# Kernel tuning notes

Hardware: AMD Instinct MI355X
Metric: run time of the kernel (lower is better)

## Reference

```python
import jax, jax.numpy as jnp
import numpy as np

B, S, IN, HID, OUT = 8, 4096, 128, 128, 1

def setup_inputs() -> dict:
    key = jax.random.key(0)
    ks = jax.random.split(key, 16)
    xav = lambda k, i, o: jax.random.normal(k, (i, o), jnp.float32) * np.sqrt(2.0 / (i + o))
    return {
        'x': jax.random.normal(ks[0], (B, S, IN), jnp.float32),
        'm1': xav(ks[1], IN, HID), 'b1': jnp.zeros((1, 1, HID), jnp.float32),
        'm2': xav(ks[2], HID, HID), 'b2': jnp.zeros((1, 1, HID), jnp.float32),
        'wq': xav(ks[3], HID, HID), 'wk': xav(ks[4], HID, HID), 'wv': xav(ks[5], HID, HID),
        'ml0': xav(ks[6], 128, 64), 'bl0': jnp.zeros((1, 1, 64), jnp.float32),
        'ml1': xav(ks[7], 64, 32), 'bl1': jnp.zeros((1, 1, 32), jnp.float32),
        'm3': xav(ks[8], 32, OUT), 'b3': jnp.zeros((1, 1, OUT), jnp.float32),
        'atten_size': 5,
    }

def reference(x, m1, b1, m2, b2, wq, wk, wv, ml0, bl0, ml1, bl1, m3, b3, atten_size):
    a = atten_size
    h = jax.nn.relu(x @ m1 + b1)
    h = jax.nn.relu(h @ m2 + b2)            # [B,S,H]
    vals = h @ wv
    pad_cfg = ((0, 0), (a, a), (0, 0))
    padded = jnp.pad(h, pad_cfg)
    padded_v = jnp.pad(vals, pad_cfg)
    # window gather via roll, matching torch.roll(padded, k, 1) for k=-a..a, then slice
    x_nei = jnp.stack([jnp.roll(padded, k, axis=1) for k in range(-a, a + 1)], axis=2)[:, a:-a]   # [B,S,W,H]
    v_nei = jnp.stack([jnp.roll(padded_v, k, axis=1) for k in range(-a, a + 1)], axis=2)[:, a:-a]
    keys = x_nei @ wk                        # [B,S,W,H]
    query = h @ wq                           # [B,S,H]
    scale = 1.0 / np.sqrt(float(HID))
    dot = jnp.einsum('bswh,bsh->bsw', keys, query) * scale
    atten_w = jax.nn.softmax(dot, axis=2)    # [B,S,W]
    o = jnp.einsum('bsw,bswh->bsh', atten_w, v_nei)
    o = jax.nn.relu(o @ ml0 + bl0)
    o = jax.nn.relu(o @ ml1 + bl1)
    o = jax.nn.sigmoid(o @ m3 + b3)          # [B,S,OUT]
    return (o, atten_w)
```

## Files before the change

kernel.cpp:

```cpp
#include <hip/hip_runtime.h>
#include <hip/hip_bf16.h>
#include <math.h>

#define SEQ 4096
#define NB 8
#define CHUNK 64
#define HALO 5
#define WIN 11
#define MROWS 80
#define AROWS 74
#define HSTR 136
#define NT 512
#define CNT 256

typedef short s16x8 __attribute__((ext_vector_type(8)));
typedef float f32x4 __attribute__((ext_vector_type(4)));

__device__ __forceinline__ unsigned short f2bf(float f) {
    return __builtin_bit_cast(unsigned short, __float2bfloat16(f));
}

#define OFF_M1  0
#define OFF_M2  16384
#define OFF_WQK 32768
#define OFF_WF  49152
#define OFF_ML1 57344
#define WS_ELEMS 59392

__global__ void convert_weights(const float* __restrict__ m1, const float* __restrict__ m2,
                                const float* __restrict__ wq, const float* __restrict__ wk,
                                const float* __restrict__ wv, const float* __restrict__ ml0,
                                const float* __restrict__ ml1, unsigned short* __restrict__ ws)
{
    int idx = blockIdx.x * CNT + threadIdx.x;
    if (idx < 16384) {
        ws[idx] = f2bf(m1[(idx & 127) * 128 + (idx >> 7)]);
    } else if (idx < 32768) {
        int r = idx - 16384;
        ws[idx] = f2bf(m2[(r & 127) * 128 + (r >> 7)]);
    } else if (idx < 49152) {
        int r = idx - 32768;
        int d = r >> 7, e = r & 127;
        const float4* qa = (const float4*)(wq + e * 128);
        const float4* ka = (const float4*)(wk + d * 128);
        float a0 = 0.f, a1 = 0.f, a2 = 0.f, a3 = 0.f;
        #pragma unroll
        for (int c = 0; c < 32; ++c) {
            float4 A = qa[c], B = ka[c];
            a0 = fmaf(A.x, B.x, a0); a1 = fmaf(A.y, B.y, a1);
            a2 = fmaf(A.z, B.z, a2); a3 = fmaf(A.w, B.w, a3);
        }
        ws[idx] = f2bf((a0 + a1 + a2 + a3) * 0.08838834764831845f);
    } else if (idx < 57344) {
        int r = idx - 49152;
        int n = r >> 7, k = r & 127;
        const float* vr = wv + k * 128;
        float a = 0.f;
        #pragma unroll
        for (int c = 0; c < 128; ++c) a = fmaf(vr[c], ml0[c * 64 + n], a);
        ws[idx] = f2bf(a);
    } else if (idx < WS_ELEMS) {
        int r = idx - 57344;
        int n = r >> 6, k = r & 63;
        ws[idx] = f2bf(ml1[k * 32 + n]);
    }
}

__device__ __forceinline__ void loadB4(s16x8 d[4], const unsigned short* __restrict__ wt,
                                       int ct, int l15, int hi)
{
    const unsigned short* p = wt + (ct * 16 + l15) * 128 + hi * 8;
    d[0] = *(const s16x8*)(p);
    d[1] = *(const s16x8*)(p + 32);
    d[2] = *(const s16x8*)(p + 64);
    d[3] = *(const s16x8*)(p + 96);
}

template<int MT, bool RELU, bool BIAS>
__device__ __forceinline__ void gemmS(const unsigned short* __restrict__ src,
                                      const s16x8 bf[4],
                                      const float* __restrict__ bias,
                                      unsigned short* __restrict__ dst,
                                      int l15, int hi, int wave)
{
    f32x4 acc[MT];
    #pragma unroll
    for (int i = 0; i < MT; ++i) acc[i] = (f32x4){0.f, 0.f, 0.f, 0.f};
    const unsigned short* arow = src + l15 * HSTR + hi * 8;
    #pragma unroll
    for (int ks = 0; ks < 4; ++ks)
        #pragma unroll
        for (int rt = 0; rt < MT; ++rt) {
            s16x8 a = *(const s16x8*)(arow + rt * 16 * HSTR + ks * 32);
            acc[rt] = __builtin_amdgcn_mfma_f32_16x16x32_bf16(a, bf[ks], acc[rt], 0, 0, 0);
        }
    const int c = wave * 16 + l15;
    const float bb = BIAS ? bias[c] : 0.f;
    #pragma unroll
    for (int rt = 0; rt < MT; ++rt)
        #pragma unroll
        for (int j = 0; j < 4; ++j) {
            float v = acc[rt][j] + bb;
            if (RELU) v = fmaxf(v, 0.f);
            dst[(rt * 16 + hi * 4 + j) * HSTR + c] = f2bf(v);
        }
}

__global__ __launch_bounds__(NT, 4)
void ExLRestSelfAtten_mfma(const float* __restrict__ x,
                           const float* __restrict__ b1, const float* __restrict__ b2,
                           const float* __restrict__ bl0, const float* __restrict__ bl1,
                           const float* __restrict__ m3, const float* __restrict__ b3,
                           const unsigned short* __restrict__ wsw,
                           float* __restrict__ out0, float* __restrict__ attw)
{
    __shared__ __align__(16) unsigned short bufA[MROWS * HSTR];
    __shared__ __align__(16) unsigned short bufB[MROWS * HSTR];
    __shared__ __align__(16) unsigned short qbuf[CHUNK * HSTR];
    __shared__ __align__(16) float sbuf[4 * 16 * 36];
    __shared__ __align__(16) float saw [CHUNK * WIN];

    unsigned short* o2b  = bufA;
    float*          fbuf = (float*)qbuf;

    const int t = threadIdx.x;
    const int lane = t & 63, wave = t >> 6;
    const int l15 = lane & 15, hi = lane >> 4;
    const int bx = blockIdx.x;
    const int b = bx >> 6;
    const int cstart = (bx & 63) * CHUNK;

    s16x8 wA[4], wB[4], wml1[2];
    loadB4(wA, wsw + OFF_M1, wave, l15, hi);

    const float* xb = x + (size_t)b * SEQ * 128;
    for (int idx = t; idx < MROWS * 32; idx += NT) {
        int r = idx >> 5, k4 = (idx & 31) << 2;
        int p = cstart - HALO + r;
        float4 v = make_float4(0.f, 0.f, 0.f, 0.f);
        if (r < AROWS && p >= 0 && p < SEQ) v = *(const float4*)(xb + (size_t)p * 128 + k4);
        ushort4 o;
        o.x = f2bf(v.x); o.y = f2bf(v.y); o.z = f2bf(v.z); o.w = f2bf(v.w);
        *(ushort4*)(bufA + r * HSTR + k4) = o;
    }
    __syncthreads();

    loadB4(wB, wsw + OFF_M2, wave, l15, hi);
    gemmS<5, true, true>(bufA, wA, b1, bufB, l15, hi, wave);
    __syncthreads();

    loadB4(wA, wsw + OFF_WQK, wave, l15, hi);
    gemmS<5, true, true>(bufB, wB, b2, bufA, l15, hi, wave);
    __syncthreads();

    loadB4(wB, wsw + OFF_WF, wave & 3, l15, hi);
    gemmS<4, false, false>(bufA + HALO * HSTR, wA, nullptr, qbuf, l15, hi, wave);
    {
        const int cg = wave & 3, rh = wave >> 2;
        const int rt0 = rh ? 3 : 0, ntr = rh ? 2 : 3;
        f32x4 acc[3];
        #pragma unroll
        for (int i = 0; i < 3; ++i) acc[i] = (f32x4){0.f, 0.f, 0.f, 0.f};
        const unsigned short* arow = bufA + (rt0 * 16 + l15) * HSTR + hi * 8;
        #pragma unroll
        for (int ks = 0; ks < 4; ++ks)
            for (int rt = 0; rt < ntr; ++rt) {
                s16x8 a = *(const s16x8*)(arow + rt * 16 * HSTR + ks * 32);
                acc[rt] = __builtin_amdgcn_mfma_f32_16x16x32_bf16(a, wB[ks], acc[rt], 0, 0, 0);
            }
        const int c = cg * 16 + l15;
        for (int rt = 0; rt < ntr; ++rt)
            #pragma unroll
            for (int j = 0; j < 4; ++j)
                bufB[((rt0 + rt) * 16 + hi * 4 + j) * HSTR + c] = f2bf(acc[rt][j]);
    }
    __syncthreads();

    {
        const unsigned short* p1 = wsw + OFF_ML1 + ((wave & 1) * 16 + l15) * 64 + hi * 8;
        wml1[0] = *(const s16x8*)(p1);
        wml1[1] = *(const s16x8*)(p1 + 32);
    }
    {
        const int rt = wave >> 1, kk = wave & 1, kt = rt + kk;
        f32x4 sacc = (f32x4){0.f, 0.f, 0.f, 0.f};
        #pragma unroll
        for (int ks = 0; ks < 4; ++ks) {
            s16x8 a  = *(const s16x8*)(qbuf + (rt * 16 + l15) * HSTR + ks * 32 + hi * 8);
            s16x8 hb = *(const s16x8*)(bufA + (kt * 16 + l15) * HSTR + ks * 32 + hi * 8);
            sacc = __builtin_amdgcn_mfma_f32_16x16x32_bf16(a, hb, sacc, 0, 0, 0);
        }
        #pragma unroll
        for (int j = 0; j < 4; ++j)
            sbuf[rt * 576 + (hi * 4 + j) * 36 + kk * 16 + l15] = sacc[j];
    }
    __syncthreads();

    if (t < CHUNK) {
        const int base = (t >> 4) * 576 + (t & 15) * 36 + (t & 15) + 10;
        float d[WIN], mx = -1e30f;
        #pragma unroll
        for (int w = 0; w < WIN; ++w) { d[w] = sbuf[base - w]; mx = fmaxf(mx, d[w]); }
        float sum = 0.f;
        #pragma unroll
        for (int w = 0; w < WIN; ++w) { d[w] = __expf(d[w] - mx); sum += d[w]; }
        float inv = 1.f / sum;
        float* ab = attw + (size_t)(b * SEQ + cstart + t) * WIN;
        #pragma unroll
        for (int w = 0; w < WIN; ++w) {
            float a = d[w] * inv;
            saw[t * WIN + w] = a;
            ab[w] = a;
        }
    }
    __syncthreads();

    {
        const int s = t >> 3, c0 = (t & 7) << 3;
        float acc[8] = {0.f, 0.f, 0.f, 0.f, 0.f, 0.f, 0.f, 0.f};
        #pragma unroll
        for (int w = 0; w < WIN; ++w) {
            float aw = saw[s * WIN + w];
            uint4 u = *(const uint4*)(bufB + (s + 10 - w) * HSTR + c0);
            unsigned uu[4] = {u.x, u.y, u.z, u.w};
            #pragma unroll
            for (int q = 0; q < 4; ++q) {
                acc[2 * q]     = fmaf(aw, __builtin_bit_cast(float, uu[q] << 16), acc[2 * q]);
                acc[2 * q + 1] = fmaf(aw, __builtin_bit_cast(float, uu[q] & 0xffff0000u), acc[2 * q + 1]);
            }
        }
        float4 bv0 = *(const float4*)(bl0 + c0);
        float4 bv1 = *(const float4*)(bl0 + c0 + 4);
        const float bb[8] = {bv0.x, bv0.y, bv0.z, bv0.w, bv1.x, bv1.y, bv1.z, bv1.w};
        unsigned short pk[8];
        #pragma unroll
        for (int i = 0; i < 8; ++i) pk[i] = f2bf(fmaxf(acc[i] + bb[i], 0.f));
        *(ushort4*)(o2b + s * 72 + c0) = *(ushort4*)(pk);
        *(ushort4*)(o2b + s * 72 + c0 + 4) = *(ushort4*)(pk + 4);
    }
    __syncthreads();

    {
        const int rt2 = wave >> 1, ct2 = wave & 1;
        f32x4 acc = (f32x4){0.f, 0.f, 0.f, 0.f};
        #pragma unroll
        for (int ks = 0; ks < 2; ++ks) {
            s16x8 a = *(const s16x8*)(o2b + (rt2 * 16 + l15) * 72 + ks * 32 + hi * 8);
            acc = __builtin_amdgcn_mfma_f32_16x16x32_bf16(a, wml1[ks], acc, 0, 0, 0);
        }
        const int c = ct2 * 16 + l15;
        const float bb = bl1[c];
        #pragma unroll
        for (int j = 0; j < 4; ++j)
            fbuf[(rt2 * 16 + hi * 4 + j) * 36 + c] = fmaxf(acc[j] + bb, 0.f);
    }
    __syncthreads();

    if (t < CHUNK) {
        float acc = b3[0];
        const float* fr = fbuf + t * 36;
        #pragma unroll
        for (int k4 = 0; k4 < 8; ++k4) {
            float4 hv = *(const float4*)(fr + k4 * 4);
            float4 mv = *(const float4*)(m3 + k4 * 4);
            acc = fmaf(hv.x, mv.x, acc); acc = fmaf(hv.y, mv.y, acc);
            acc = fmaf(hv.z, mv.z, acc); acc = fmaf(hv.w, mv.w, acc);
        }
        out0[(size_t)b * SEQ + cstart + t] = 1.f / (1.f + __expf(-acc));
    }
}

extern "C" void kernel_launch(void* const* d_in, const int* in_sizes, int n_in,
                              void* d_out, int out_size, void* d_ws, size_t ws_size,
                              hipStream_t stream)
{
    const float* x   = (const float*)d_in[0];
    const float* m1  = (const float*)d_in[1];
    const float* b1  = (const float*)d_in[2];
    const float* m2  = (const float*)d_in[3];
    const float* b2  = (const float*)d_in[4];
    const float* wq  = (const float*)d_in[5];
    const float* wk  = (const float*)d_in[6];
    const float* wv  = (const float*)d_in[7];
    const float* ml0 = (const float*)d_in[8];
    const float* bl0 = (const float*)d_in[9];
    const float* ml1 = (const float*)d_in[10];
    const float* bl1 = (const float*)d_in[11];
    const float* m3  = (const float*)d_in[12];
    const float* b3  = (const float*)d_in[13];

    float* out0 = (float*)d_out;
    float* attw = out0 + (size_t)NB * SEQ;

    unsigned short* wsw = (unsigned short*)d_ws;
    convert_weights<<<(WS_ELEMS + CNT - 1) / CNT, CNT, 0, stream>>>(
        m1, m2, wq, wk, wv, ml0, ml1, wsw);
    ExLRestSelfAtten_mfma<<<NB * (SEQ / CHUNK), NT, 0, stream>>>(
        x, b1, b2, bl0, bl1, m3, b3, wsw, out0, attw);
}
```

Baseline: 25.23 us.

## Fuse x load into first GEMM, banded scores with in-wave softmax, fused tail

The first layer now reads x straight from global memory into MFMA A-fragments, converting to bf16 in registers instead of staging through shared memory, which removes one barrier and one LDS round trip. The score computation keeps only the 11-wide diagonal band in a small per-wave buffer, and the softmax runs in the same waves, which removes a barrier and the larger scores buffer. The final ml1 GEMM and the m3 dot product plus sigmoid are fused using wave shuffles, dropping another barrier and the fbuf staging. V is stored with a narrower stride to cut LDS use. The trade-off is that only some waves are active in the later phases, and the direct global loads may coalesce less well than the old staged copy.

Measured after the change: 42.92 us. 70.1% more time.

```diff
diff --git a/kernel.cpp b/kernel.cpp
--- a/kernel.cpp
+++ b/kernel.cpp
@@ -8,8 +8,8 @@
 #define HALO 5
 #define WIN 11
 #define MROWS 80
-#define AROWS 74
 #define HSTR 136
+#define VSTR 72
 #define NT 512
 #define CNT 256
 
@@ -117,11 +117,11 @@
     __shared__ __align__(16) unsigned short bufA[MROWS * HSTR];
     __shared__ __align__(16) unsigned short bufB[MROWS * HSTR];
     __shared__ __align__(16) unsigned short qbuf[CHUNK * HSTR];
-    __shared__ __align__(16) float sbuf[4 * 16 * 36];
+    __shared__ __align__(16) float sband[4 * 16 * 12];
     __shared__ __align__(16) float saw [CHUNK * WIN];
 
-    unsigned short* o2b  = bufA;
-    float*          fbuf = (float*)qbuf;
+    unsigned short* vhb = bufA;
+    unsigned short* o2b = qbuf;
 
     const int t = threadIdx.x;
     const int lane = t & 63, wave = t >> 6;
@@ -130,38 +130,57 @@
     const int b = bx >> 6;
     const int cstart = (bx & 63) * CHUNK;
 
-    s16x8 wA[4], wB[4], wml1[2];
+    s16x8 wA[4], wB[4];
     loadB4(wA, wsw + OFF_M1, wave, l15, hi);
-
-    const float* xb = x + (size_t)b * SEQ * 128;
-    for (int idx = t; idx < MROWS * 32; idx += NT) {
-        int r = idx >> 5, k4 = (idx & 31) << 2;
-        int p = cstart - HALO + r;
-        float4 v = make_float4(0.f, 0.f, 0.f, 0.f);
-        if (r < AROWS && p >= 0 && p < SEQ) v = *(const float4*)(xb + (size_t)p * 128 + k4);
-        ushort4 o;
-        o.x = f2bf(v.x); o.y = f2bf(v.y); o.z = f2bf(v.z); o.w = f2bf(v.w);
-        *(ushort4*)(bufA + r * HSTR + k4) = o;
-    }
-    __syncthreads();
-
     loadB4(wB, wsw + OFF_M2, wave, l15, hi);
-    gemmS<5, true, true>(bufA, wA, b1, bufB, l15, hi, wave);
-    __syncthreads();
-
+
+    {
+        const float* xb = x + (size_t)b * SEQ * 128;
+        f32x4 acc[5];
+        #pragma unroll
+        for (int i = 0; i < 5; ++i) acc[i] = (f32x4){0.f, 0.f, 0.f, 0.f};
+        int prow[5]; bool pval[5];
+        #pragma unroll
+        for (int rt = 0; rt < 5; ++rt) {
+            int p = cstart - HALO + rt * 16 + l15;
+            pval[rt] = (p >= 0 && p < SEQ);
+            prow[rt] = pval[rt] ? p : 0;
+        }
+        #pragma unroll
+        for (int ks = 0; ks < 4; ++ks)
+            #pragma unroll
+            for (int rt = 0; rt < 5; ++rt) {
+                const float4* xp = (const float4*)(xb + (size_t)prow[rt] * 128 + ks * 32 + hi * 8);
+                float4 lo = xp[0], hp = xp[1];
+                if (!pval[rt]) { lo = make_float4(0.f,0.f,0.f,0.f); hp = lo; }
+                union { s16x8 v; unsigned short u[8]; } A;
+                A.u[0]=f2bf(lo.x); A.u[1]=f2bf(lo.y); A.u[2]=f2bf(lo.z); A.u[3]=f2bf(lo.w);
+                A.u[4]=f2bf(hp.x); A.u[5]=f2bf(hp.y); A.u[6]=f2bf(hp.z); A.u[7]=f2bf(hp.w);
+                acc[rt] = __builtin_amdgcn_mfma_f32_16x16x32_bf16(A.v, wA[ks], acc[rt], 0, 0, 0);
+            }
+        const int c = wave * 16 + l15;
+        const float bb = b1[c];
+        #pragma unroll
+        for (int rt = 0; rt < 5; ++rt)
+            #pragma unroll
+            for (int j = 0; j < 4; ++j)
+                bufA[(rt * 16 + hi * 4 + j) * HSTR + c] = f2bf(fmaxf(acc[rt][j] + bb, 0.f));
+    }
     loadB4(wA, wsw + OFF_WQK, wave, l15, hi);
-    gemmS<5, true, true>(bufB, wB, b2, bufA, l15, hi, wave);
-    __syncthreads();
-
+    __syncthreads();
+
+    gemmS<5, true, true>(bufA, wB, b2, bufB, l15, hi, wave);
     loadB4(wB, wsw + OFF_WF, wave & 3, l15, hi);
-    gemmS<4, false, false>(bufA + HALO * HSTR, wA, nullptr, qbuf, l15, hi, wave);
+    __syncthreads();
+
+    gemmS<4, false, false>(bufB + HALO * HSTR, wA, nullptr, qbuf, l15, hi, wave);
     {
         const int cg = wave & 3, rh = wave >> 2;
         const int rt0 = rh ? 3 : 0, ntr = rh ? 2 : 3;
         f32x4 acc[3];
         #pragma unroll
         for (int i = 0; i < 3; ++i) acc[i] = (f32x4){0.f, 0.f, 0.f, 0.f};
-        const unsigned short* arow = bufA + (rt0 * 16 + l15) * HSTR + hi * 8;
+        const unsigned short* arow = bufB + (rt0 * 16 + l15) * HSTR + hi * 8;
         #pragma unroll
         for (int ks = 0; ks < 4; ++ks)
             for (int rt = 0; rt < ntr; ++rt) {
@@ -172,56 +191,73 @@
         for (int rt = 0; rt < ntr; ++rt)
             #pragma unroll
             for (int j = 0; j < 4; ++j)
-                bufB[((rt0 + rt) * 16 + hi * 4 + j) * HSTR + c] = f2bf(acc[rt][j]);
-    }
-    __syncthreads();
-
-    {
-        const unsigned short* p1 = wsw + OFF_ML1 + ((wave & 1) * 16 + l15) * 64 + hi * 8;
-        wml1[0] = *(const s16x8*)(p1);
-        wml1[1] = *(const s16x8*)(p1 + 32);
-    }
-    {
-        const int rt = wave >> 1, kk = wave & 1, kt = rt + kk;
-        f32x4 sacc = (f32x4){0.f, 0.f, 0.f, 0.f};
+                vhb[((rt0 + rt) * 16 + hi * 4 + j) * VSTR + c] = f2bf(acc[rt][j]);
+    }
+    __syncthreads();
+
+    if (wave < 4) {
+        const int rt = wave;
+        f32x4 s0 = (f32x4){0.f,0.f,0.f,0.f}, s1 = s0;
         #pragma unroll
         for (int ks = 0; ks < 4; ++ks) {
             s16x8 a  = *(const s16x8*)(qbuf + (rt * 16 + l15) * HSTR + ks * 32 + hi * 8);
-            s16x8 hb = *(const s16x8*)(bufA + (kt * 16 + l15) * HSTR + ks * 32 + hi * 8);
-            sacc = __builtin_amdgcn_mfma_f32_16x16x32_bf16(a, hb, sacc, 0, 0, 0);
-        }
-        #pragma unroll
-        for (int j = 0; j < 4; ++j)
-            sbuf[rt * 576 + (hi * 4 + j) * 36 + kk * 16 + l15] = sacc[j];
-    }
-    __syncthreads();
-
-    if (t < CHUNK) {
-        const int base = (t >> 4) * 576 + (t & 15) * 36 + (t & 15) + 10;
-        float d[WIN], mx = -1e30f;
-        #pragma unroll
-        for (int w = 0; w < WIN; ++w) { d[w] = sbuf[base - w]; mx = fmaxf(mx, d[w]); }
-        float sum = 0.f;
-        #pragma unroll
-        for (int w = 0; w < WIN; ++w) { d[w] = __expf(d[w] - mx); sum += d[w]; }
-        float inv = 1.f / sum;
-        float* ab = attw + (size_t)(b * SEQ + cstart + t) * WIN;
-        #pragma unroll
-        for (int w = 0; w < WIN; ++w) {
-            float a = d[w] * inv;
-            saw[t * WIN + w] = a;
-            ab[w] = a;
-        }
-    }
-    __syncthreads();
-
+            s16x8 h0 = *(const s16x8*)(bufB + (rt * 16 + l15) * HSTR + ks * 32 + hi * 8);
+            s16x8 h1f= *(const s16x8*)(bufB + ((rt + 1) * 16 + l15) * HSTR + ks * 32 + hi * 8);
+            s0 = __builtin_amdgcn_mfma_f32_16x16x32_bf16(a, h0, s0, 0, 0, 0);
+            s1 = __builtin_amdgcn_mfma_f32_16x16x32_bf16(a, h1f, s1, 0, 0, 0);
+        }
+        float* sb = sband + wave * 192;
+        const int rl = hi * 4;
+        #pragma unroll
+        for (int j = 0; j < 4; ++j) {
+            int w = rl + j + 10 - l15;
+            if (w >= 0 && w <= 10) sb[(rl + j) * 12 + w] = s0[j];
+        }
+        #pragma unroll
+        for (int j = 0; j < 4; ++j) {
+            int w = rl + j - 6 - l15;
+            if (w >= 0) sb[(rl + j) * 12 + w] = s1[j];
+        }
+        __builtin_amdgcn_s_waitcnt(0);
+        if (hi == 0) {
+            const float* sr = sb + l15 * 12;
+            float d[WIN], mx = -1e30f;
+            #pragma unroll
+            for (int w = 0; w < WIN; ++w) { d[w] = sr[w]; mx = fmaxf(mx, d[w]); }
+            float sum = 0.f;
+            #pragma unroll
+            for (int w = 0; w < WIN; ++w) { d[w] = __expf(d[w] - mx); sum += d[w]; }
+            float inv = 1.f / sum;
+            const int s = rt * 16 + l15;
+            float* ab = attw + (size_t)(b * SEQ + cstart + s) * WIN;
+            #pragma unroll
+            for (int w = 0; w < WIN; ++w) {
+                float a = d[w] * inv;
+                saw[s * WIN + w] = a;
+                ab[w] = a;
+            }
+        }
+    }
+    __syncthreads();
+
+    s16x8 wml1[2][2];
+    float bl1a = 0.f, bl1b = 0.f, m3a = 0.f, m3b = 0.f, b3v = 0.f;
+    if (wave < 2) {
+        const unsigned short* p0 = wsw + OFF_ML1 + l15 * 64 + hi * 8;
+        const unsigned short* p1 = wsw + OFF_ML1 + (16 + l15) * 64 + hi * 8;
+        wml1[0][0] = *(const s16x8*)(p0); wml1[0][1] = *(const s16x8*)(p0 + 32);
+        wml1[1][0] = *(const s16x8*)(p1); wml1[1][1] = *(const s16x8*)(p1 + 32);
+        bl1a = bl1[l15]; bl1b = bl1[16 + l15];
+        m3a = m3[l15];   m3b = m3[16 + l15];
+        b3v = b3[0];
+    }
     {
         const int s = t >> 3, c0 = (t & 7) << 3;
-        float acc[8] = {0.f, 0.f, 0.f, 0.f, 0.f, 0.f, 0.f, 0.f};
+        float acc[8] = {0.f,0.f,0.f,0.f,0.f,0.f,0.f,0.f};
         #pragma unroll
         for (int w = 0; w < WIN; ++w) {
             float aw = saw[s * WIN + w];
-            uint4 u = *(const uint4*)(bufB + (s + 10 - w) * HSTR + c0);
+            uint4 u = *(const uint4*)(vhb + (s + 10 - w) * VSTR + c0);
             unsigned uu[4] = {u.x, u.y, u.z, u.w};
             #pragma unroll
             for (int q = 0; q < 4; ++q) {
@@ -235,38 +271,42 @@
         unsigned short pk[8];
         #pragma unroll
         for (int i = 0; i < 8; ++i) pk[i] = f2bf(fmaxf(acc[i] + bb[i], 0.f));
-        *(ushort4*)(o2b + s * 72 + c0) = *(ushort4*)(pk);
-        *(ushort4*)(o2b + s * 72 + c0 + 4) = *(ushort4*)(pk + 4);
-    }
-    __syncthreads();
-
-    {
-        const int rt2 = wave >> 1, ct2 = wave & 1;
-        f32x4 acc = (f32x4){0.f, 0.f, 0.f, 0.f};
-        #pragma unroll
-        for (int ks = 0; ks < 2; ++ks) {
-            s16x8 a = *(const s16x8*)(o2b + (rt2 * 16 + l15) * 72 + ks * 32 + hi * 8);
-            acc = __builtin_amdgcn_mfma_f32_16x16x32_bf16(a, wml1[ks], acc, 0, 0, 0);
-        }
-        const int c = ct2 * 16 + l15;
-        const float bb = bl1[c];
-        #pragma unroll
-        for (int j = 0; j < 4; ++j)
-            fbuf[(rt2 * 16 + hi * 4 + j) * 36 + c] = fmaxf(acc[j] + bb, 0.f);
-    }
-    __syncthreads();
-
-    if (t < CHUNK) {
-        float acc = b3[0];
-        const float* fr = fbuf + t * 36;
-        #pragma unroll
-        for (int k4 = 0; k4 < 8; ++k4) {
-            float4 hv = *(const float4*)(fr + k4 * 4);
-            float4 mv = *(const float4*)(m3 + k4 * 4);
-            acc = fmaf(hv.x, mv.x, acc); acc = fmaf(hv.y, mv.y, acc);
-            acc = fmaf(hv.z, mv.z, acc); acc = fmaf(hv.w, mv.w, acc);
-        }
-        out0[(size_t)b * SEQ + cstart + t] = 1.f / (1.f + __expf(-acc));
+        uint4 ov;
+        ov.x = pk[0] | ((unsigned)pk[1] << 16); ov.y = pk[2] | ((unsigned)pk[3] << 16);
+        ov.z = pk[4] | ((unsigned)pk[5] << 16); ov.w = pk[6] | ((unsigned)pk[7] << 16);
+        *(uint4*)(o2b + s * VSTR + c0) = ov;
+    }
+    __syncthreads();
+
+    if (wave < 2) {
+        f32x4 acc[2][2];
+        #pragma unroll
+        for (int i = 0; i < 2; ++i) { acc[i][0] = (f32x4){0.f,0.f,0.f,0.f}; acc[i][1] = acc[i][0]; }
+        #pragma unroll
+        for (int ri = 0; ri < 2; ++ri) {
+            const int rt = wave * 2 + ri;
+            #pragma unroll
+            for (int ks = 0; ks < 2; ++ks) {
+                s16x8 a = *(const s16x8*)(o2b + (rt * 16 + l15) * VSTR + ks * 32 + hi * 8);
+                acc[ri][0] = __builtin_amdgcn_mfma_f32_16x16x32_bf16(a, wml1[0][ks], acc[ri][0], 0, 0, 0);
+                acc[ri][1] = __builtin_amdgcn_mfma_f32_16x16x32_bf16(a, wml1[1][ks], acc[ri][1], 0, 0, 0);
+            }
+        }
+        float* ob = out0 + (size_t)b * SEQ + cstart;
+        #pragma unroll
+        for (int ri = 0; ri < 2; ++ri)
+            #pragma unroll
+            for (int j = 0; j < 4; ++j) {
+                float v0 = fmaxf(acc[ri][0][j] + bl1a, 0.f);
+                float v1 = fmaxf(acc[ri][1][j] + bl1b, 0.f);
+                float con = v0 * m3a + v1 * m3b;
+                con += __shfl_xor(con, 1, 64);
+                con += __shfl_xor(con, 2, 64);
+                con += __shfl_xor(con, 4, 64);
+                con += __shfl_xor(con, 8, 64);
+                if (l15 == 0)
+                    ob[(wave * 2 + ri) * 16 + hi * 4 + j] = 1.f / (1.f + __expf(-(con + b3v)));
+            }
     }
 }
 
```

## Fuse score band, softmax, and final MLP head into per-wave stages with fewer barriers

Applied to the files above, without the earlier changes.

Score computation now runs on four waves that each compute both key tiles for a 16-row query tile. Each wave writes only the 11-wide diagonal band and runs the softmax itself after a wave-local LDS wait, so one block barrier goes away. The final ml1 GEMM and the 32-to-1 head are fused with shuffle reductions, which removes the fbuf round trip and another barrier. In exchange, half the waves sit idle during these stages, and correctness depends on the wave-local lgkmcnt wait being enough to order LDS writes before reads within a wave.

New measurement: 26.99 us. 7.0% more time.

```diff
diff --git a/kernel.cpp b/kernel.cpp
--- a/kernel.cpp
+++ b/kernel.cpp
@@ -10,11 +10,14 @@
 #define MROWS 80
 #define AROWS 74
 #define HSTR 136
+#define VSTR 72
 #define NT 512
 #define CNT 256
 
 typedef short s16x8 __attribute__((ext_vector_type(8)));
 typedef float f32x4 __attribute__((ext_vector_type(4)));
+
+#define WAVE_SYNC() asm volatile("s_waitcnt lgkmcnt(0)" ::: "memory")
 
 __device__ __forceinline__ unsigned short f2bf(float f) {
     return __builtin_bit_cast(unsigned short, __float2bfloat16(f));
@@ -117,20 +120,19 @@
     __shared__ __align__(16) unsigned short bufA[MROWS * HSTR];
     __shared__ __align__(16) unsigned short bufB[MROWS * HSTR];
     __shared__ __align__(16) unsigned short qbuf[CHUNK * HSTR];
-    __shared__ __align__(16) float sbuf[4 * 16 * 36];
+    __shared__ __align__(16) float sband[4 * 16 * 12];
     __shared__ __align__(16) float saw [CHUNK * WIN];
 
-    unsigned short* o2b  = bufA;
-    float*          fbuf = (float*)qbuf;
+    unsigned short* o2b = bufA;
 
     const int t = threadIdx.x;
     const int lane = t & 63, wave = t >> 6;
-    const int l15 = lane & 15, hi = lane >> 4;
+    const int l15 = lane & 15, hi = lane >> 4, rl = hi * 4;
     const int bx = blockIdx.x;
     const int b = bx >> 6;
     const int cstart = (bx & 63) * CHUNK;
 
-    s16x8 wA[4], wB[4], wml1[2];
+    s16x8 wA[4], wB[4];
     loadB4(wA, wsw + OFF_M1, wave, l15, hi);
 
     const float* xb = x + (size_t)b * SEQ * 128;
@@ -176,48 +178,65 @@
     }
     __syncthreads();
 
-    {
-        const unsigned short* p1 = wsw + OFF_ML1 + ((wave & 1) * 16 + l15) * 64 + hi * 8;
-        wml1[0] = *(const s16x8*)(p1);
-        wml1[1] = *(const s16x8*)(p1 + 32);
-    }
-    {
-        const int rt = wave >> 1, kk = wave & 1, kt = rt + kk;
-        f32x4 sacc = (f32x4){0.f, 0.f, 0.f, 0.f};
+    s16x8 wml1[2][2];
+    float bl1a, bl1b, m3a, m3b, b3v;
+    if (wave < 4) {
+        const int rt = wave;
+        s16x8 aq[4];
+        #pragma unroll
+        for (int ks = 0; ks < 4; ++ks)
+            aq[ks] = *(const s16x8*)(qbuf + (rt * 16 + l15) * HSTR + ks * 32 + hi * 8);
+        f32x4 s0 = (f32x4){0.f, 0.f, 0.f, 0.f}, s1 = s0;
         #pragma unroll
         for (int ks = 0; ks < 4; ++ks) {
-            s16x8 a  = *(const s16x8*)(qbuf + (rt * 16 + l15) * HSTR + ks * 32 + hi * 8);
-            s16x8 hb = *(const s16x8*)(bufA + (kt * 16 + l15) * HSTR + ks * 32 + hi * 8);
-            sacc = __builtin_amdgcn_mfma_f32_16x16x32_bf16(a, hb, sacc, 0, 0, 0);
-        }
-        #pragma unroll
-        for (int j = 0; j < 4; ++j)
-            sbuf[rt * 576 + (hi * 4 + j) * 36 + kk * 16 + l15] = sacc[j];
-    }
-    __syncthreads();
-
-    if (t < CHUNK) {
-        const int base = (t >> 4) * 576 + (t & 15) * 36 + (t & 15) + 10;
-        float d[WIN], mx = -1e30f;
-        #pragma unroll
-        for (int w = 0; w < WIN; ++w) { d[w] = sbuf[base - w]; mx = fmaxf(mx, d[w]); }
-        float sum = 0.f;
-        #pragma unroll
-        for (int w = 0; w < WIN; ++w) { d[w] = __expf(d[w] - mx); sum += d[w]; }
-        float inv = 1.f / sum;
-        float* ab = attw + (size_t)(b * SEQ + cstart + t) * WIN;
-        #pragma unroll
-        for (int w = 0; w < WIN; ++w) {
-            float a = d[w] * inv;
-            saw[t * WIN + w] = a;
-            ab[w] = a;
-        }
+            s16x8 k0 = *(const s16x8*)(bufA + (rt * 16 + l15) * HSTR + ks * 32 + hi * 8);
+            s16x8 k1 = *(const s16x8*)(bufA + ((rt + 1) * 16 + l15) * HSTR + ks * 32 + hi * 8);
+            s0 = __builtin_amdgcn_mfma_f32_16x16x32_bf16(aq[ks], k0, s0, 0, 0, 0);
+            s1 = __builtin_amdgcn_mfma_f32_16x16x32_bf16(aq[ks], k1, s1, 0, 0, 0);
+        }
+        float* sb = sband + rt * 192;
+        #pragma unroll
+        for (int j = 0; j < 4; ++j) {
+            int w0 = rl + j + 10 - l15;
+            if (w0 >= 0 && w0 <= 10) sb[(rl + j) * 12 + w0] = s0[j];
+        }
+        #pragma unroll
+        for (int j = 0; j < 4; ++j) {
+            int w1 = rl + j - 6 - l15;
+            if (w1 >= 0 && w1 <= 10) sb[(rl + j) * 12 + w1] = s1[j];
+        }
+        WAVE_SYNC();
+        if (hi == 0) {
+            const float* sr = sb + l15 * 12;
+            float d[WIN], mx = -1e30f;
+            #pragma unroll
+            for (int w = 0; w < WIN; ++w) { d[w] = sr[w]; mx = fmaxf(mx, d[w]); }
+            float sum = 0.f;
+            #pragma unroll
+            for (int w = 0; w < WIN; ++w) { d[w] = __expf(d[w] - mx); sum += d[w]; }
+            float inv = 1.f / sum;
+            const int s = rt * 16 + l15;
+            float* ab = attw + (size_t)(b * SEQ + cstart + s) * WIN;
+            #pragma unroll
+            for (int w = 0; w < WIN; ++w) {
+                float a = d[w] * inv;
+                saw[s * WIN + w] = a;
+                ab[w] = a;
+            }
+        }
+        const unsigned short* p0 = wsw + OFF_ML1 + l15 * 64 + hi * 8;
+        const unsigned short* p1 = wsw + OFF_ML1 + (16 + l15) * 64 + hi * 8;
+        wml1[0][0] = *(const s16x8*)(p0); wml1[0][1] = *(const s16x8*)(p0 + 32);
+        wml1[1][0] = *(const s16x8*)(p1); wml1[1][1] = *(const s16x8*)(p1 + 32);
+        bl1a = bl1[l15]; bl1b = bl1[16 + l15];
+        m3a = m3[l15];   m3b = m3[16 + l15];
+        b3v = b3[0];
     }
     __syncthreads();
 
     {
         const int s = t >> 3, c0 = (t & 7) << 3;
-        float acc[8] = {0.f, 0.f, 0.f, 0.f, 0.f, 0.f, 0.f, 0.f};
+        float acc[8] = {0.f,0.f,0.f,0.f,0.f,0.f,0.f,0.f};
         #pragma unroll
         for (int w = 0; w < WIN; ++w) {
             float aw = saw[s * WIN + w];
@@ -235,38 +254,38 @@
         unsigned short pk[8];
         #pragma unroll
         for (int i = 0; i < 8; ++i) pk[i] = f2bf(fmaxf(acc[i] + bb[i], 0.f));
-        *(ushort4*)(o2b + s * 72 + c0) = *(ushort4*)(pk);
-        *(ushort4*)(o2b + s * 72 + c0 + 4) = *(ushort4*)(pk + 4);
-    }
-    __syncthreads();
-
-    {
-        const int rt2 = wave >> 1, ct2 = wave & 1;
-        f32x4 acc = (f32x4){0.f, 0.f, 0.f, 0.f};
+        uint4 ov;
+        ov.x = pk[0] | ((unsigned)pk[1] << 16); ov.y = pk[2] | ((unsigned)pk[3] << 16);
+        ov.z = pk[4] | ((unsigned)pk[5] << 16); ov.w = pk[6] | ((unsigned)pk[7] << 16);
+        *(uint4*)(o2b + s * VSTR + c0) = ov;
+    }
+    __syncthreads();
+
+    if (wave < 4) {
+        const int ot = wave;
+        s16x8 ao[2];
+        #pragma unroll
+        for (int ks = 0; ks < 2; ++ks)
+            ao[ks] = *(const s16x8*)(o2b + (ot * 16 + l15) * VSTR + ks * 32 + hi * 8);
+        f32x4 h0 = (f32x4){0.f, 0.f, 0.f, 0.f}, h1 = h0;
         #pragma unroll
         for (int ks = 0; ks < 2; ++ks) {
-            s16x8 a = *(const s16x8*)(o2b + (rt2 * 16 + l15) * 72 + ks * 32 + hi * 8);
-            acc = __builtin_amdgcn_mfma_f32_16x16x32_bf16(a, wml1[ks], acc, 0, 0, 0);
-        }
-        const int c = ct2 * 16 + l15;
-        const float bb = bl1[c];
-        #pragma unroll
-        for (int j = 0; j < 4; ++j)
-            fbuf[(rt2 * 16 + hi * 4 + j) * 36 + c] = fmaxf(acc[j] + bb, 0.f);
-    }
-    __syncthreads();
-
-    if (t < CHUNK) {
-        float acc = b3[0];
-        const float* fr = fbuf + t * 36;
-        #pragma unroll
-        for (int k4 = 0; k4 < 8; ++k4) {
-            float4 hv = *(const float4*)(fr + k4 * 4);
-            float4 mv = *(const float4*)(m3 + k4 * 4);
-            acc = fmaf(hv.x, mv.x, acc); acc = fmaf(hv.y, mv.y, acc);
-            acc = fmaf(hv.z, mv.z, acc); acc = fmaf(hv.w, mv.w, acc);
-        }
-        out0[(size_t)b * SEQ + cstart + t] = 1.f / (1.f + __expf(-acc));
+            h0 = __builtin_amdgcn_mfma_f32_16x16x32_bf16(ao[ks], wml1[0][ks], h0, 0, 0, 0);
+            h1 = __builtin_amdgcn_mfma_f32_16x16x32_bf16(ao[ks], wml1[1][ks], h1, 0, 0, 0);
+        }
+        float* ob = out0 + (size_t)b * SEQ + cstart + ot * 16;
+        #pragma unroll
+        for (int j = 0; j < 4; ++j) {
+            float v0 = fmaxf(h0[j] + bl1a, 0.f);
+            float v1 = fmaxf(h1[j] + bl1b, 0.f);
+            float con = v0 * m3a + v1 * m3b;
+            con += __shfl_xor(con, 1, 64);
+            con += __shfl_xor(con, 2, 64);
+            con += __shfl_xor(con, 4, 64);
+            con += __shfl_xor(con, 8, 64);
+            if (l15 == 0)
+                ob[rl + j] = 1.f / (1.f + __expf(-(con + b3v)));
+        }
     }
 }
 
```
